# Kernel tuning notes

Measured on AMD Instinct MI355X. Metric: run time of the kernel, lower is better.

## Reference

```python
import jax, jax.numpy as jnp
import numpy as np
from jax import lax

IN_CH = 512
OUT_CH = 512
KERNEL = 3
STYLE_DIM = 512
BATCH = 8
HW = 64
EPS = 1e-08
LR_MUL = 1.0


def setup_inputs() -> dict:
    key = jax.random.key(0)
    k1, k2, k3, k4 = jax.random.split(key, 4)
    x = jax.random.normal(k1, (BATCH, IN_CH, HW, HW), dtype=jnp.float32)
    style = jax.random.normal(k2, (BATCH, STYLE_DIM), dtype=jnp.float32)
    weight = jax.random.normal(k3, (1, OUT_CH, IN_CH, KERNEL, KERNEL), dtype=jnp.float32)
    mod_weight = jax.random.normal(k4, (IN_CH, STYLE_DIM), dtype=jnp.float32)
    mod_bias = jnp.ones((IN_CH,), dtype=jnp.float32)  # bias_init=1
    return {"x": x, "style": style, "weight": weight,
            "mod_weight": mod_weight, "mod_bias": mod_bias}


def reference(x, style, weight, mod_weight, mod_bias):
    batch, in_ch, h, w_dim = x.shape
    conv_scale = 1.0 / np.sqrt(in_ch * KERNEL * KERNEL)
    lin_scale = 1.0 / np.sqrt(STYLE_DIM) * LR_MUL

    # EqualizedLinear modulation: style -> per-channel scale, shape (B, in_ch)
    s = style @ (mod_weight * lin_scale).T + mod_bias * LR_MUL

    # Modulate: (B, out, in, k, k)
    w = conv_scale * weight * s[:, None, :, None, None]
    # Demodulate
    demod = lax.rsqrt(jnp.sum(w * w, axis=(2, 3, 4)) + EPS)  # (B, out)
    w = w * demod[:, :, None, None, None]

    pad = KERNEL // 2

    def conv_one(xi, wi):
        # xi: (in, H, W), wi: (out, in, k, k)
        return lax.conv_general_dilated(
            xi[None], wi, window_strides=(1, 1),
            padding=[(pad, pad), (pad, pad)],
            dimension_numbers=("NCHW", "OIHW", "NCHW"))[0]

    out = jax.vmap(conv_one)(x, w)  # (B, out, H, W)
    return out
```

## Files before the change

### kernel.cpp

```cpp
#include <hip/hip_runtime.h>
#include <hip/hip_bf16.h>
#include <cstdint>

#define IN_CH 512
#define OUT_CH 512
#define STYLE_DIM 512
#define BATCH 8
#define HW 64

typedef __bf16 bf16x8 __attribute__((ext_vector_type(8)));
typedef float f32x16 __attribute__((ext_vector_type(16)));

__device__ __forceinline__ void gload_lds16(const void* g, void* l) {
  __builtin_amdgcn_global_load_lds(
      (const __attribute__((address_space(1))) unsigned int*)g,
      (__attribute__((address_space(3))) unsigned int*)l,
      16, 0, 0);
}

#define WAITV(N) asm volatile("s_waitcnt vmcnt(" #N ")" ::: "memory")
#define BARRIER() do { asm volatile("" ::: "memory"); __builtin_amdgcn_s_barrier(); \
                       asm volatile("" ::: "memory"); } while (0)

__global__ void k_style(const float* __restrict__ style, const float* __restrict__ modw,
                        const float* __restrict__ modb, float* __restrict__ s_out) {
  __shared__ float st[BATCH * STYLE_DIM];
  const int tid = threadIdx.x;
  for (int i = tid; i < BATCH * STYLE_DIM; i += 256) st[i] = style[i];
  __syncthreads();
  const int ic = blockIdx.x * 4 + (tid >> 6);
  const int l = tid & 63;
  const float* mr = modw + (size_t)ic * STYLE_DIM + l * 8;
  float m[8];
  #pragma unroll
  for (int j = 0; j < 8; ++j) m[j] = mr[j];
  float accs[8];
  #pragma unroll
  for (int b = 0; b < 8; ++b) {
    const float* sb = st + b * STYLE_DIM + l * 8;
    float a = 0.f;
    #pragma unroll
    for (int j = 0; j < 8; ++j) a += m[j] * sb[j];
    accs[b] = a;
  }
  #pragma unroll
  for (int off = 32; off; off >>= 1) {
    #pragma unroll
    for (int b = 0; b < 8; ++b) accs[b] += __shfl_down(accs[b], off, 64);
  }
  if (l == 0) {
    #pragma unroll
    for (int b = 0; b < 8; ++b)
      s_out[b * IN_CH + ic] = accs[b] * 0.04419417382415922f + modb[ic];
  }
}

__global__ void k_wprep(const float* __restrict__ w, float* __restrict__ wsq,
                        __bf16* __restrict__ wb) {
  const int idx = blockIdx.x * 256 + threadIdx.x;
  const int oc = idx >> 9, ic = idx & 511;
  const float* p = w + ((size_t)oc * IN_CH + ic) * 9;
  const int icw = ic ^ ((oc & 7) << 3);
  float sum = 0.f;
  #pragma unroll
  for (int t = 0; t < 9; ++t) {
    float v = p[t];
    sum += v * v;
    wb[((size_t)(t * OUT_CH) + oc) * IN_CH + icw] = (__bf16)v;
  }
  wsq[oc * IN_CH + ic] = sum;
}

__global__ void k_demod(const float* __restrict__ s, const float* __restrict__ wsq,
                        float* __restrict__ scale) {
  const int oc = blockIdx.x;
  const int l = threadIdx.x;
  const float* wr = wsq + (size_t)oc * IN_CH + l * 8;
  float w8[8];
  #pragma unroll
  for (int j = 0; j < 8; ++j) w8[j] = wr[j];
  #pragma unroll
  for (int b = 0; b < 8; ++b) {
    const float* sb = s + b * IN_CH + l * 8;
    float acc = 0.f;
    #pragma unroll
    for (int j = 0; j < 8; ++j) { float sv = sb[j]; acc += sv * sv * w8[j]; }
    #pragma unroll
    for (int off = 32; off; off >>= 1) acc += __shfl_down(acc, off, 64);
    if (l == 0)
      scale[b * OUT_CH + oc] =
          rsqrtf(acc * (1.0f / 4608.0f) + 1e-8f) * 0.014731391274719732f;
  }
}

__global__ void k_xprep(const float* __restrict__ x, const float* __restrict__ s,
                        __bf16* __restrict__ xg) {
  const int b = blockIdx.x >> 6, y = blockIdx.x & 63;
  const int w = threadIdx.x >> 6, lane = threadIdx.x & 63;
  const float* sr = s + b * IN_CH;
  #pragma unroll
  for (int it = 0; it < 8; ++it) {
    const int ug = it * 8 + w;
    bf16x8 pk;
    #pragma unroll
    for (int j = 0; j < 8; ++j) {
      const int ic = ug * 8 + j;
      pk[j] = (__bf16)(x[(((size_t)(b * IN_CH) + ic) * HW + y) * HW + lane] * sr[ic]);
    }
    *(bf16x8*)(xg + ((((size_t)(b * 64 + ug) * HW + y) * HW + lane) * 8)) = pk;
  }
}

__global__ __launch_bounds__(512, 2) void k_conv(
    const __bf16* __restrict__ Wg,
    const __bf16* __restrict__ Xg,
    const float* __restrict__ scale,
    float* __restrict__ out)
{
  __shared__ __attribute__((aligned(16))) __bf16 Xs[6 * 66 * 64];
  __shared__ __attribute__((aligned(16))) __bf16 Wl[3][256 * 64];
  __shared__ __attribute__((aligned(16))) __bf16 Dump[4096];

  const int tid = threadIdx.x;
  const int lane = tid & 63;
  const int wid = tid >> 6;
  const int wm = wid >> 2;
  const int wn = wid & 3;
  const int ln31 = lane & 31;
  const int laneK = lane >> 5;

  const int bid0 = blockIdx.x;
  const int bid = (bid0 & 7) * 32 + (bid0 >> 3);
  const int octile = bid & 1;
  const int ptile = (bid >> 1) & 15;
  const int b = bid >> 5;
  const int oc0 = octile * 256;
  const int r0 = ptile * 4;

  auto stage_w = [&](int chunkv, int tapv, int bsel) {
    const int ic0 = chunkv * 64;
    #pragma unroll
    for (int i = 0; i < 4; ++i) {
      const int sidx = tid + 512 * i;
      const int oc = sidx >> 3, u = sidx & 7;
      gload_lds16(Wg + (((size_t)(tapv * OUT_CH) + oc0 + oc) * IN_CH + ic0 + u * 8),
                  &Wl[bsel][oc * 64 + u * 8]);
    }
  };
  auto stage_x = [&](int chunkv) {
    const int col = tid >> 3;
    const int u = tid & 7;
    const int ug = chunkv * 8 + (u ^ ((col + 1) & 7));
    #pragma unroll
    for (int j = 0; j < 6; ++j) {
      const int y = r0 - 1 + j;
      const bool ok = (y >= 0 && y < HW);
      const int yc = ok ? y : 0;
      void* dst = ok ? (void*)&Xs[(j * 66 + col + 1) * 64 + u * 8]
                     : (void*)&Dump[tid * 8];
      gload_lds16(Xg + ((((size_t)(b * 64 + ug) * HW + yc) * HW + col) * 8), dst);
    }
  };

  {
    float4 z = {0.f, 0.f, 0.f, 0.f};
    float4* p = (float4*)Xs;
    for (int i = tid; i < 6 * 66 * 64 / 8; i += 512) p[i] = z;
  }
  __syncthreads();
  stage_x(0);
  stage_w(0, 0, 0);
  stage_w(0, 1, 1);

  const int akey8 = (ln31 & 7) << 3;
  const int kb = laneK * 8;
  const __bf16* wbase[3];
  #pragma unroll
  for (int i = 0; i < 3; ++i) wbase[i] = &Wl[i][(128 * wm + ln31) * 64];
  const __bf16* xbt[9];
  #pragma unroll
  for (int t = 0; t < 9; ++t) {
    const int dy = t / 3 - 1, dx = t % 3 - 1;
    xbt[t] = &Xs[((wn + 1 + dy) * 66 + (ln31 + 1 + dx)) * 64];
  }
  int aoffe[4];
  #pragma unroll
  for (int ks = 0; ks < 4; ++ks) aoffe[ks] = (ks * 16 + kb) ^ akey8;
  int bele[3][4];
  #pragma unroll
  for (int dxi = 0; dxi < 3; ++dxi) {
    const int bkey8 = ((ln31 + dxi) & 7) << 3;
    #pragma unroll
    for (int ks = 0; ks < 4; ++ks) bele[dxi][ks] = (ks * 16 + kb) ^ bkey8;
  }

  f32x16 acc[4][2] = {};
  bf16x8 Aa[4], Ab[2], Ba[4], Bb[2];

#define RDA(P, KS, BUF) { _Pragma("unroll") for (int mf = 0; mf < 4; ++mf) \
    P##a[mf] = *(const bf16x8*)(wbase[BUF] + aoffe[KS] + mf * 2048); }
#define RDB(P, TAP, KS) { const __bf16* p_ = xbt[TAP] + bele[(TAP) % 3][KS]; \
    P##b[0] = *(const bf16x8*)p_; P##b[1] = *(const bf16x8*)(p_ + 2048); }
#define MM(P) { __builtin_amdgcn_s_setprio(1); \
    _Pragma("unroll") for (int mf = 0; mf < 4; ++mf) { \
      acc[mf][0] = __builtin_amdgcn_mfma_f32_32x32x16_bf16(P##a[mf], P##b[0], acc[mf][0], 0, 0, 0); \
      acc[mf][1] = __builtin_amdgcn_mfma_f32_32x32x16_bf16(P##a[mf], P##b[1], acc[mf][1], 0, 0, 0); } \
    __builtin_amdgcn_s_setprio(0); }

#define TAPBODY(T) { \
    WAITV(0); BARRIER(); \
    if ((T) == 0) { RDA(A, 0, 0) RDB(A, 0, 0) }             \
    RDA(B, 1, (T) % 3) RDB(B, (T), 1)                        \
    MM(A)                                                    \
    if ((T) <= 6)      stage_w(c,     (T) + 2, ((T) + 2) % 3); \
    else if (c < 7)    stage_w(c + 1, (T) - 7, ((T) + 2) % 3); \
    RDA(A, 2, (T) % 3) RDB(A, (T), 2)                        \
    MM(B)                                                    \
    RDA(B, 3, (T) % 3) RDB(B, (T), 3)                        \
    MM(A)                                                    \
    if ((T) < 8) { RDA(A, 0, ((T) + 1) % 3) RDB(A, (T) + 1, 0) }   \
    MM(B)                                                    \
    if ((T) == 8) { BARRIER(); if (c < 7) stage_x(c + 1); } \
  }

  #pragma unroll 1
  for (int c = 0; c < 8; ++c) {
    TAPBODY(0) TAPBODY(1) TAPBODY(2)
    TAPBODY(3) TAPBODY(4) TAPBODY(5)
    TAPBODY(6) TAPBODY(7) TAPBODY(8)
  }

  const int y = r0 + wn;
  #pragma unroll
  for (int mf = 0; mf < 4; ++mf) {
    #pragma unroll
    for (int reg = 0; reg < 16; ++reg) {
      const int rowid = (reg & 3) + 8 * (reg >> 2) + 4 * laneK;
      const int oc = oc0 + 128 * wm + 32 * mf + rowid;
      const float sc = scale[b * OUT_CH + oc];
      float* op = out + (((size_t)(b * OUT_CH + oc) * HW + y) * HW) + ln31;
      op[0] = acc[mf][0][reg] * sc;
      op[32] = acc[mf][1][reg] * sc;
    }
  }
}

extern "C" void kernel_launch(void* const* d_in, const int* in_sizes, int n_in,
                              void* d_out, int out_size, void* d_ws, size_t ws_size,
                              hipStream_t stream) {
  const float* x      = (const float*)d_in[0];
  const float* style  = (const float*)d_in[1];
  const float* weight = (const float*)d_in[2];
  const float* modw   = (const float*)d_in[3];
  const float* modb   = (const float*)d_in[4];
  float* out = (float*)d_out;

  char* ws = (char*)d_ws;
  float*  s_buf = (float*)(ws + 0);
  float*  scale = (float*)(ws + 16384);
  float*  wsq   = (float*)(ws + 32768);
  __bf16* wb    = (__bf16*)(ws + 32768 + 1048576);
  __bf16* xg    = (__bf16*)(ws + 32768 + 1048576 + 9 * OUT_CH * IN_CH * 2);

  k_style<<<128, 256, 0, stream>>>(style, modw, modb, s_buf);
  k_wprep<<<1024, 256, 0, stream>>>(weight, wsq, wb);
  k_demod<<<512, 64, 0, stream>>>(s_buf, wsq, scale);
  k_xprep<<<BATCH * HW, 512, 0, stream>>>(x, s_buf, xg);
  k_conv<<<256, 512, 0, stream>>>(wb, xg, scale, out);
}
```

Baseline: 191.6 us.

## Relax per-tap vmcnt wait and restructure weight staging and LDS reads

Each tap now waits with vmcnt(4) instead of vmcnt(0), so the newest weight stage can stay in flight across the barrier. Weight staging for later taps, and the next chunk's X and tap-1 weights, are now issued after the tap's MFMAs rather than mid-tap. The hand-written A/B register double-buffering of LDS fragments is replaced by a plain per-k-step load-then-MFMA loop, leaving instruction scheduling to the compiler. The LDS dump buffer for out-of-range rows is shrunk. The aim is to hide global-to-LDS latency, at the risk of exposing LDS read latency that the old software prefetch hid.

Result: faster. 170.8 us (-10.9%).

```diff
diff --git a/kernel.cpp b/kernel.cpp
--- a/kernel.cpp
+++ b/kernel.cpp
@@ -119,7 +119,7 @@
 {
   __shared__ __attribute__((aligned(16))) __bf16 Xs[6 * 66 * 64];
   __shared__ __attribute__((aligned(16))) __bf16 Wl[3][256 * 64];
-  __shared__ __attribute__((aligned(16))) __bf16 Dump[4096];
+  __shared__ __attribute__((aligned(16))) __bf16 Dump[1024];
 
   const int tid = threadIdx.x;
   const int lane = tid & 63;
@@ -157,7 +157,7 @@
       const bool ok = (y >= 0 && y < HW);
       const int yc = ok ? y : 0;
       void* dst = ok ? (void*)&Xs[(j * 66 + col + 1) * 64 + u * 8]
-                     : (void*)&Dump[tid * 8];
+                     : (void*)&Dump[(tid & 127) * 8];
       gload_lds16(Xg + ((((size_t)(b * 64 + ug) * HW + yc) * HW + col) * 8), dst);
     }
   };
@@ -172,17 +172,8 @@
   stage_w(0, 0, 0);
   stage_w(0, 1, 1);
 
+  const int kb = laneK * 8;
   const int akey8 = (ln31 & 7) << 3;
-  const int kb = laneK * 8;
-  const __bf16* wbase[3];
-  #pragma unroll
-  for (int i = 0; i < 3; ++i) wbase[i] = &Wl[i][(128 * wm + ln31) * 64];
-  const __bf16* xbt[9];
-  #pragma unroll
-  for (int t = 0; t < 9; ++t) {
-    const int dy = t / 3 - 1, dx = t % 3 - 1;
-    xbt[t] = &Xs[((wn + 1 + dy) * 66 + (ln31 + 1 + dx)) * 64];
-  }
   int aoffe[4];
   #pragma unroll
   for (int ks = 0; ks < 4; ++ks) aoffe[ks] = (ks * 16 + kb) ^ akey8;
@@ -193,34 +184,42 @@
     #pragma unroll
     for (int ks = 0; ks < 4; ++ks) bele[dxi][ks] = (ks * 16 + kb) ^ bkey8;
   }
+  const __bf16* __restrict__ wbp0 = &Wl[0][(128 * wm + ln31) * 64];
+  const __bf16* __restrict__ wbp1 = wbp0 + 256 * 64;
+  const __bf16* __restrict__ wbp2 = wbp1 + 256 * 64;
+  const __bf16* __restrict__ xwb = &Xs[((wn + 1) * 66 + (ln31 + 1)) * 64];
 
   f32x16 acc[4][2] = {};
-  bf16x8 Aa[4], Ab[2], Ba[4], Bb[2];
-
-#define RDA(P, KS, BUF) { _Pragma("unroll") for (int mf = 0; mf < 4; ++mf) \
-    P##a[mf] = *(const bf16x8*)(wbase[BUF] + aoffe[KS] + mf * 2048); }
-#define RDB(P, TAP, KS) { const __bf16* p_ = xbt[TAP] + bele[(TAP) % 3][KS]; \
-    P##b[0] = *(const bf16x8*)p_; P##b[1] = *(const bf16x8*)(p_ + 2048); }
-#define MM(P) { __builtin_amdgcn_s_setprio(1); \
-    _Pragma("unroll") for (int mf = 0; mf < 4; ++mf) { \
-      acc[mf][0] = __builtin_amdgcn_mfma_f32_32x32x16_bf16(P##a[mf], P##b[0], acc[mf][0], 0, 0, 0); \
-      acc[mf][1] = __builtin_amdgcn_mfma_f32_32x32x16_bf16(P##a[mf], P##b[1], acc[mf][1], 0, 0, 0); } \
-    __builtin_amdgcn_s_setprio(0); }
 
 #define TAPBODY(T) { \
-    WAITV(0); BARRIER(); \
-    if ((T) == 0) { RDA(A, 0, 0) RDB(A, 0, 0) }             \
-    RDA(B, 1, (T) % 3) RDB(B, (T), 1)                        \
-    MM(A)                                                    \
-    if ((T) <= 6)      stage_w(c,     (T) + 2, ((T) + 2) % 3); \
-    else if (c < 7)    stage_w(c + 1, (T) - 7, ((T) + 2) % 3); \
-    RDA(A, 2, (T) % 3) RDB(A, (T), 2)                        \
-    MM(B)                                                    \
-    RDA(B, 3, (T) % 3) RDB(B, (T), 3)                        \
-    MM(A)                                                    \
-    if ((T) < 8) { RDA(A, 0, ((T) + 1) % 3) RDB(A, (T) + 1, 0) }   \
-    MM(B)                                                    \
-    if ((T) == 8) { BARRIER(); if (c < 7) stage_x(c + 1); } \
+    if ((T) == 8 && c == 7) { WAITV(0); } else { WAITV(4); } \
+    BARRIER(); \
+    const __bf16* __restrict__ wbase = ((T) % 3 == 0) ? wbp0 : ((T) % 3 == 1) ? wbp1 : wbp2; \
+    const __bf16* __restrict__ xb0 = xwb + (((T) / 3 - 1) * 66 + ((T) % 3 - 1)) * 64; \
+    _Pragma("unroll") \
+    for (int ks = 0; ks < 4; ++ks) { \
+      const int ael = aoffe[ks]; \
+      const int bel = bele[(T) % 3][ks]; \
+      bf16x8 av[4], bv[2]; \
+      _Pragma("unroll") \
+      for (int mf = 0; mf < 4; ++mf) av[mf] = *(const bf16x8*)(wbase + mf * 2048 + ael); \
+      bv[0] = *(const bf16x8*)(xb0 + bel); \
+      bv[1] = *(const bf16x8*)(xb0 + 32 * 64 + bel); \
+      __builtin_amdgcn_s_setprio(1); \
+      _Pragma("unroll") \
+      for (int mf = 0; mf < 4; ++mf) { \
+        acc[mf][0] = __builtin_amdgcn_mfma_f32_32x32x16_bf16(av[mf], bv[0], acc[mf][0], 0, 0, 0); \
+        acc[mf][1] = __builtin_amdgcn_mfma_f32_32x32x16_bf16(av[mf], bv[1], acc[mf][1], 0, 0, 0); \
+      } \
+      __builtin_amdgcn_s_setprio(0); \
+    } \
+    if ((T) == 8) { \
+      if (c < 7) { BARRIER(); stage_x(c + 1); stage_w(c + 1, 1, 1); } \
+    } else if ((T) <= 6) { \
+      stage_w(c, (T) + 2, ((T) + 2) % 3); \
+    } else {  \
+      if (c < 7) stage_w(c + 1, 0, 0); \
+    } \
   }
 
   #pragma unroll 1
```
